# Kernel optimization log

Hardware: AMD Instinct MI355X
Metric: run time of the kernel (lower is better)

The kernel has to match this reference:

```python
import jax, jax.numpy as jnp
import numpy as np

NUM_HEADS = 12
HEAD_DIM = 64
NPT = 1  # num_prefix_tokens

def _rot(x):
    # pairs (x0,x1) -> (-x1, x0), matching timm's rot()
    x2 = x.reshape(*x.shape[:-1], -1, 2)
    r = jnp.stack([-x2[..., 1], x2[..., 0]], axis=-1)
    return r.reshape(x.shape)

def _apply_rope_cat(x, rope):
    # rope: [N_rot, 2*hd] = sin||cos concatenated
    sin, cos = jnp.split(rope, 2, axis=-1)
    return x * cos + _rot(x) * sin

def setup_inputs() -> dict:
    key = jax.random.key(0)
    ks = jax.random.split(key, 7)
    B, N, C = 8, 4097, 768
    hd = HEAD_DIM
    x = jax.random.normal(ks[0], (B, N, C), jnp.float32)
    rope = jax.random.normal(ks[1], (N - NPT, 2 * hd), jnp.float32)
    qkv_w = jax.random.normal(ks[2], (3 * C, C), jnp.float32) * (C ** -0.5)
    q_bias = jax.random.normal(ks[3], (C,), jnp.float32) * 0.02
    v_bias = jax.random.normal(ks[4], (C,), jnp.float32) * 0.02
    proj_w = jax.random.normal(ks[5], (C, C), jnp.float32) * (C ** -0.5)
    proj_b = jax.random.normal(ks[6], (C,), jnp.float32) * 0.02
    return dict(x=x, rope=rope, qkv_w=qkv_w, q_bias=q_bias, v_bias=v_bias,
                proj_w=proj_w, proj_b=proj_b)

def reference(x, rope, qkv_w, q_bias, v_bias, proj_w, proj_b):
    B, N, C = x.shape
    H, hd = NUM_HEADS, HEAD_DIM
    # fused QKV with k_bias fixed at zero (non-trainable buffer)
    bias = jnp.concatenate([q_bias, jnp.zeros_like(q_bias), v_bias])
    qkv = x @ qkv_w.T + bias                            # [B,N,3C]
    qkv = qkv.reshape(B, N, 3, H, hd).transpose(2, 0, 3, 1, 4)
    q, k, v = qkv[0], qkv[1], qkv[2]                    # [B,H,N,hd]
    # RoPE on all tokens except the prefix (CLS) token
    q = jnp.concatenate([q[:, :, :NPT], _apply_rope_cat(q[:, :, NPT:], rope)], axis=2)
    k = jnp.concatenate([k[:, :, :NPT], _apply_rope_cat(k[:, :, NPT:], rope)], axis=2)
    # linear attention: kv = K^T V, then Q @ kv, normalized by hd*N
    kv = jnp.einsum('bhnd,bhne->bhde', k, v)            # [B,H,hd,hd]
    out = jnp.einsum('bhnd,bhde->bhne', q, kv) / hd / N # [B,H,N,hd]
    out = out.transpose(0, 2, 1, 3).reshape(B, N, C)
    return out @ proj_w.T + proj_b
```

## Files before the change

### kernel.cpp

```cpp
#include <hip/hip_runtime.h>
#include <hip/hip_bf16.h>

typedef __attribute__((ext_vector_type(8))) short short8;
typedef __attribute__((ext_vector_type(4))) float f32x4;

#define B_    8
#define N_    4097
#define C_    768
#define M_TOT (B_*N_)
#define K3    (3*C_)
#define CHUNKS 16
#define NSTEP 24

__device__ __forceinline__ float bf2f(unsigned short u) {
  union { unsigned int i; float f; } x; x.i = ((unsigned int)u) << 16; return x.f;
}
__device__ __forceinline__ unsigned short f2bf(float f) {
  union { float f; unsigned int i; } x; x.f = f;
  unsigned int i = x.i + 0x7fffu + ((x.i >> 16) & 1u);
  return (unsigned short)(i >> 16);
}
__device__ __forceinline__ void gload16(const void* g, void* l) {
  __builtin_amdgcn_global_load_lds(
      (const __attribute__((address_space(1))) void*)g,
      (__attribute__((address_space(3))) void*)l, 16, 0, 0);
}

__global__ __launch_bounds__(256) void cvt_kernel(const float* __restrict__ inx,
                                                  unsigned short* __restrict__ outx,
                                                  const float* __restrict__ inw,
                                                  unsigned short* __restrict__ outw,
                                                  long n4x, long n4tot) {
  long i = (long)blockIdx.x * blockDim.x + threadIdx.x;
  long stride = (long)gridDim.x * blockDim.x;
  for (; i < n4tot; i += stride) {
    const float4* src; ushort4* dst; long j;
    if (i < n4x) { src = (const float4*)inx; dst = (ushort4*)outx; j = i; }
    else         { src = (const float4*)inw; dst = (ushort4*)outw; j = i - n4x; }
    float4 v = src[j];
    ushort4 o;
    o.x = f2bf(v.x); o.y = f2bf(v.y); o.z = f2bf(v.z); o.w = f2bf(v.w);
    dst[j] = o;
  }
}

__global__ __launch_bounds__(512, 4) void gemm_qkv_rope(
    const unsigned short* __restrict__ A,
    const unsigned short* __restrict__ Bw,
    const float* __restrict__ rope,
    const float* __restrict__ qb,
    const float* __restrict__ vb,
    unsigned short* __restrict__ qkv)
{
  __shared__ __align__(16) char L[3*24576];
  const int tid  = threadIdx.x;
  const int wave = tid >> 6, lane = tid & 63;
  const int lr = lane & 15, lk = lane >> 4;
  const int wm = wave >> 2, wn = wave & 3;

  const int o = blockIdx.x;
  const int xcd = o & 7, loc = o >> 3;
  const int tile = (xcd < 1 ? xcd*290 : 290 + (xcd-1)*289) + loc;
  const int m0 = (tile / 9) * 128;
  const int n0 = (tile % 9) * 256;

  const int arow = tid >> 2, achk = tid & 3;
  const int am = min(m0 + arow, M_TOT-1);
  const unsigned short* gA  = A  + (long)am*768 + achk*8;
  const unsigned short* gB1 = Bw + (long)(n0 + arow)*768 + achk*8;
  const unsigned short* gB2 = Bw + (long)(n0 + arow + 128)*768 + achk*8;
  const int dA  = wave*1024;
  const int dB1 = 8192  + wave*1024;
  const int dB2 = 16384 + wave*1024;

  const int abase = (wm*64 + lr)*64 + lk*16;
  const int bbase = 8192 + (wn*64 + lr)*64 + lk*16;

  f32x4 acc[4][4];
#pragma unroll
  for (int i = 0; i < 4; ++i)
#pragma unroll
    for (int j = 0; j < 4; ++j) acc[i][j] = (f32x4){0.f,0.f,0.f,0.f};

  auto STAGE = [&](int buf, int kk) {
    char* sb = L + buf*24576;
    gload16(gA  + kk, sb + dA);
    gload16(gB1 + kk, sb + dB1);
    gload16(gB2 + kk, sb + dB2);
  };
  auto COMPUTE = [&](int buf) {
    const char* sb = L + buf*24576;
    short8 af[4], bfr[4];
#pragma unroll
    for (int mi = 0; mi < 4; ++mi)
      af[mi] = *(const short8*)(sb + abase + mi*1024);
#pragma unroll
    for (int ni = 0; ni < 4; ++ni)
      bfr[ni] = *(const short8*)(sb + bbase + ni*1024);
#pragma unroll
    for (int mi = 0; mi < 4; ++mi)
#pragma unroll
      for (int ni = 0; ni < 4; ++ni)
        acc[mi][ni] = __builtin_amdgcn_mfma_f32_16x16x32_bf16(af[mi], bfr[ni], acc[mi][ni], 0, 0, 0);
  };

  STAGE(0, 0);
  STAGE(1, 32);
  asm volatile("s_waitcnt vmcnt(3)" ::: "memory");
  __builtin_amdgcn_s_barrier();
  __builtin_amdgcn_sched_barrier(0);

  int cur = 0;
  for (int tt = 0; tt < NSTEP-2; ++tt) {
    int stg = cur + 2; if (stg >= 3) stg -= 3;
    STAGE(stg, (tt+2)*32);
    COMPUTE(cur);
    asm volatile("s_waitcnt vmcnt(3)" ::: "memory");
    __builtin_amdgcn_sched_barrier(0);
    __builtin_amdgcn_s_barrier();
    __builtin_amdgcn_sched_barrier(0);
    cur = (cur + 1 == 3) ? 0 : cur + 1;
  }
  COMPUTE(cur);
  asm volatile("s_waitcnt vmcnt(0)" ::: "memory");
  __builtin_amdgcn_sched_barrier(0);
  __builtin_amdgcn_s_barrier();
  __builtin_amdgcn_sched_barrier(0);
  cur = (cur + 1 == 3) ? 0 : cur + 1;
  COMPUTE(cur);

  const int which = n0 / 768;
  unsigned short* plane = qkv + (long)which*M_TOT*768;

  float biasv[4]; int withv[4]; int dv[4];
#pragma unroll
  for (int ni = 0; ni < 4; ++ni) {
    const int gc = n0 + wn*64 + ni*16 + lr;
    const int within = gc - which*768;
    withv[ni] = within;
    dv[ni] = within & 63;
    biasv[ni] = (which == 0) ? qb[within] : (which == 2 ? vb[within] : 0.f);
  }

  if (which == 2) {
#pragma unroll
    for (int mi = 0; mi < 4; ++mi)
#pragma unroll
      for (int r = 0; r < 4; ++r) {
        const int gm = m0 + wm*64 + mi*16 + lk*4 + r;
        if (gm < M_TOT) {
#pragma unroll
          for (int ni = 0; ni < 4; ++ni)
            plane[(long)gm*768 + withv[ni]] = f2bf(acc[mi][ni][r] + biasv[ni]);
        }
      }
  } else {
#pragma unroll
    for (int mi = 0; mi < 4; ++mi) {
#pragma unroll
      for (int r = 0; r < 4; ++r) {
        const int gm = m0 + wm*64 + mi*16 + lk*4 + r;
        const int ntok = gm % 4097;
        const bool valid = gm < M_TOT;
        const bool dorope = (ntok > 0) && valid;
        const float* rp = rope + (long)(ntok - 1)*128;
#pragma unroll
        for (int ni = 0; ni < 4; ++ni) {
          float v = acc[mi][ni][r] + biasv[ni];
          float pair = __shfl_xor(v, 1);
          float vo = v;
          if (dorope) {
            const float s = rp[dv[ni]], c = rp[64 + dv[ni]];
            const float rot = (dv[ni] & 1) ? pair : -pair;
            vo = v*c + rot*s;
          }
          if (valid) plane[(long)gm*768 + withv[ni]] = f2bf(vo);
        }
      }
    }
  }
}

__global__ __launch_bounds__(256) void kv_partial_kernel(
    const unsigned short* __restrict__ qkv, float* __restrict__ part)
{
  const int bh = blockIdx.y;
  const int b = bh / 12, h = bh % 12;
  const int chunk = blockIdx.x;
  const int per = (N_ + CHUNKS - 1) / CHUNKS;
  const int nst = chunk * per;
  const int nen = min(nst + per, N_);
  const unsigned short* Kpl = qkv + (long)M_TOT*768 + ((long)b*N_)*768 + h*64;
  const unsigned short* Vpl = qkv + (long)2*M_TOT*768 + ((long)b*N_)*768 + h*64;
  __shared__ unsigned short Kl[2][32*64];
  __shared__ unsigned short Vl[2][32*64];
  const int t = threadIdx.x;
  const int ty = t >> 4, tx = t & 15;
  const int lrow = t >> 3, lpc = t & 7;
  float acc[4][4] = {};

  {
    const int cnt0 = min(32, nen - nst);
    if (lrow < cnt0) {
      *(uint4*)(Kl[0] + lrow*64 + lpc*8) = *(const uint4*)(Kpl + (long)(nst + lrow)*768 + lpc*8);
      *(uint4*)(Vl[0] + lrow*64 + lpc*8) = *(const uint4*)(Vpl + (long)(nst + lrow)*768 + lpc*8);
    }
  }
  int cur = 0;
  for (int nb = nst; nb < nen; nb += 32) {
    uint4 kn, vn; int cntn = 0;
    const int nxt = nb + 32;
    if (nxt < nen) {
      cntn = min(32, nen - nxt);
      if (lrow < cntn) {
        kn = *(const uint4*)(Kpl + (long)(nxt + lrow)*768 + lpc*8);
        vn = *(const uint4*)(Vpl + (long)(nxt + lrow)*768 + lpc*8);
      }
    }
    __syncthreads();
    const int cnt = min(32, nen - nb);
#pragma unroll 2
    for (int i = 0; i < cnt; ++i) {
      const ushort4 ku = *(const ushort4*)(Kl[cur] + i*64 + ty*4);
      const ushort4 vu = *(const ushort4*)(Vl[cur] + i*64 + tx*4);
      float kf[4] = {bf2f(ku.x), bf2f(ku.y), bf2f(ku.z), bf2f(ku.w)};
      float vf[4] = {bf2f(vu.x), bf2f(vu.y), bf2f(vu.z), bf2f(vu.w)};
#pragma unroll
      for (int a = 0; a < 4; ++a)
#pragma unroll
        for (int e = 0; e < 4; ++e) acc[a][e] += kf[a]*vf[e];
    }
    __syncthreads();
    if (nxt < nen && lrow < cntn) {
      *(uint4*)(Kl[cur^1] + lrow*64 + lpc*8) = kn;
      *(uint4*)(Vl[cur^1] + lrow*64 + lpc*8) = vn;
    }
    cur ^= 1;
  }
  float* dst = part + ((long)chunk*96 + bh)*4096 + (ty*4)*64 + tx*4;
#pragma unroll
  for (int a = 0; a < 4; ++a)
#pragma unroll
    for (int e = 0; e < 4; ++e) dst[a*64 + e] = acc[a][e];
}

__global__ __launch_bounds__(256) void mcomb_kernel(const float* __restrict__ part,
                                                    const float* __restrict__ pw,
                                                    unsigned short* __restrict__ McT) {
  const int blk = blockIdx.x;
  const int cs = blk & 3;
  const int h  = (blk >> 2) % 12;
  const int b  = blk / 48;
  const int bh = b*12 + h;
  __shared__ float kvs[64][65];
  const int t = threadIdx.x;
  const int d_own = t >> 2;
  const int eg = (t & 3) * 16;

  float4 a0 = {0,0,0,0}, a1 = {0,0,0,0}, a2 = {0,0,0,0}, a3 = {0,0,0,0};
  const float4* p4 = (const float4*)part;
#pragma unroll
  for (int ch = 0; ch < CHUNKS; ++ch) {
    const long base = ((long)ch*96 + bh)*1024 + d_own*16 + (t & 3)*4;
    float4 v0 = p4[base+0], v1 = p4[base+1], v2 = p4[base+2], v3 = p4[base+3];
    a0.x += v0.x; a0.y += v0.y; a0.z += v0.z; a0.w += v0.w;
    a1.x += v1.x; a1.y += v1.y; a1.z += v1.z; a1.w += v1.w;
    a2.x += v2.x; a2.y += v2.y; a2.z += v2.z; a2.w += v2.w;
    a3.x += v3.x; a3.y += v3.y; a3.z += v3.z; a3.w += v3.w;
  }
  kvs[eg+ 0][d_own] = a0.x; kvs[eg+ 1][d_own] = a0.y; kvs[eg+ 2][d_own] = a0.z; kvs[eg+ 3][d_own] = a0.w;
  kvs[eg+ 4][d_own] = a1.x; kvs[eg+ 5][d_own] = a1.y; kvs[eg+ 6][d_own] = a1.z; kvs[eg+ 7][d_own] = a1.w;
  kvs[eg+ 8][d_own] = a2.x; kvs[eg+ 9][d_own] = a2.y; kvs[eg+10][d_own] = a2.z; kvs[eg+11][d_own] = a2.w;
  kvs[eg+12][d_own] = a3.x; kvs[eg+13][d_own] = a3.y; kvs[eg+14][d_own] = a3.z; kvs[eg+15][d_own] = a3.w;
  __syncthreads();

  const int lane = t & 63;
  const int w    = t >> 6;
  float kvcol[64];
#pragma unroll
  for (int e = 0; e < 64; ++e) kvcol[e] = kvs[e][lane];

  const float scale = (float)(1.0/(64.0*4097.0));
  const int cbase = cs*192 + w*48;
  for (int i = 0; i < 48; ++i) {
    const int c = cbase + i;
    const float* pwrow = pw + (long)c*768 + h*64;
    float s = 0.f;
#pragma unroll
    for (int e = 0; e < 64; ++e) s += pwrow[e] * kvcol[e];
    McT[((long)b*768 + c)*768 + h*64 + lane] = f2bf(s * scale);
  }
}

__global__ __launch_bounds__(512, 4) void gemm_final(
    const unsigned short* __restrict__ qkv,
    const unsigned short* __restrict__ McT,
    const float* __restrict__ pb,
    float* __restrict__ out)
{
  __shared__ __align__(16) char L[3*24576];
  const int tid  = threadIdx.x;
  const int wave = tid >> 6, lane = tid & 63;
  const int lr = lane & 15, lk = lane >> 4;
  const int wm = wave >> 2, wn = wave & 3;

  const int o = blockIdx.x;
  const int xcd = o & 7, loc = o >> 3;
  const int b  = xcd;
  const int mt = loc / 3, ct = loc % 3;
  const int m0 = mt * 128;
  const int c0 = ct * 256;

  const int arow = tid >> 2, achk = tid & 3;
  const int am = min(m0 + arow, N_-1);
  const unsigned short* gA  = qkv + ((long)b*N_ + am)*768 + achk*8;
  const unsigned short* Bb  = McT + (long)b*768*768;
  const unsigned short* gB1 = Bb + (long)(c0 + arow)*768 + achk*8;
  const unsigned short* gB2 = Bb + (long)(c0 + arow + 128)*768 + achk*8;
  const int dA  = wave*1024;
  const int dB1 = 8192  + wave*1024;
  const int dB2 = 16384 + wave*1024;

  const int abase = (wm*64 + lr)*64 + lk*16;
  const int bbase = 8192 + (wn*64 + lr)*64 + lk*16;

  f32x4 acc[4][4];
#pragma unroll
  for (int i = 0; i < 4; ++i)
#pragma unroll
    for (int j = 0; j < 4; ++j) acc[i][j] = (f32x4){0.f,0.f,0.f,0.f};

  auto STAGE = [&](int buf, int kk) {
    char* sb = L + buf*24576;
    gload16(gA  + kk, sb + dA);
    gload16(gB1 + kk, sb + dB1);
    gload16(gB2 + kk, sb + dB2);
  };
  auto COMPUTE = [&](int buf) {
    const char* sb = L + buf*24576;
    short8 af[4], bfr[4];
#pragma unroll
    for (int mi = 0; mi < 4; ++mi)
      af[mi] = *(const short8*)(sb + abase + mi*1024);
#pragma unroll
    for (int ni = 0; ni < 4; ++ni)
      bfr[ni] = *(const short8*)(sb + bbase + ni*1024);
#pragma unroll
    for (int mi = 0; mi < 4; ++mi)
#pragma unroll
      for (int ni = 0; ni < 4; ++ni)
        acc[mi][ni] = __builtin_amdgcn_mfma_f32_16x16x32_bf16(af[mi], bfr[ni], acc[mi][ni], 0, 0, 0);
  };

  STAGE(0, 0);
  STAGE(1, 32);
  asm volatile("s_waitcnt vmcnt(3)" ::: "memory");
  __builtin_amdgcn_s_barrier();
  __builtin_amdgcn_sched_barrier(0);

  int cur = 0;
  for (int tt = 0; tt < NSTEP-2; ++tt) {
    int stg = cur + 2; if (stg >= 3) stg -= 3;
    STAGE(stg, (tt+2)*32);
    COMPUTE(cur);
    asm volatile("s_waitcnt vmcnt(3)" ::: "memory");
    __builtin_amdgcn_sched_barrier(0);
    __builtin_amdgcn_s_barrier();
    __builtin_amdgcn_sched_barrier(0);
    cur = (cur + 1 == 3) ? 0 : cur + 1;
  }
  COMPUTE(cur);
  asm volatile("s_waitcnt vmcnt(0)" ::: "memory");
  __builtin_amdgcn_sched_barrier(0);
  __builtin_amdgcn_s_barrier();
  __builtin_amdgcn_sched_barrier(0);
  cur = (cur + 1 == 3) ? 0 : cur + 1;
  COMPUTE(cur);

#pragma unroll
  for (int mi = 0; mi < 4; ++mi) {
#pragma unroll
    for (int ni = 0; ni < 4; ++ni) {
      const int gc = c0 + wn*64 + ni*16 + lr;
      const float bias = pb[gc];
#pragma unroll
      for (int r = 0; r < 4; ++r) {
        const int tok = m0 + wm*64 + mi*16 + lk*4 + r;
        if (tok < N_)
          out[((long)b*N_ + tok)*768 + gc] = acc[mi][ni][r] + bias;
      }
    }
  }
}

extern "C" void kernel_launch(void* const* d_in, const int* in_sizes, int n_in,
                              void* d_out, int out_size, void* d_ws, size_t ws_size,
                              hipStream_t stream) {
  const float* x      = (const float*)d_in[0];
  const float* rope   = (const float*)d_in[1];
  const float* qkv_w  = (const float*)d_in[2];
  const float* q_bias = (const float*)d_in[3];
  const float* v_bias = (const float*)d_in[4];
  const float* proj_w = (const float*)d_in[5];
  const float* proj_b = (const float*)d_in[6];
  float* out = (float*)d_out;

  char* w0 = (char*)d_ws;
  unsigned short* x_bf  = (unsigned short*)w0;
  unsigned short* wq_bf = (unsigned short*)(w0 + 50343936);
  unsigned short* qkv   = (unsigned short*)(w0 + 50343936 + 3538944);
  float*          part  = (float*)w0;
  unsigned short* McT   = (unsigned short*)(w0 + 25165824 + 1572864);

  const long n4x = (long)M_TOT*768/4;
  const long n4w = (long)K3*768/4;
  cvt_kernel<<<2048, 256, 0, stream>>>(x, x_bf, qkv_w, wq_bf, n4x, n4x + n4w);

  gemm_qkv_rope<<<2313, 512, 0, stream>>>(x_bf, wq_bf, rope, q_bias, v_bias, qkv);

  kv_partial_kernel<<<dim3(CHUNKS, 96), 256, 0, stream>>>(qkv, part);
  mcomb_kernel<<<384, 256, 0, stream>>>(part, proj_w, McT);

  gemm_final<<<792, 512, 0, stream>>>(qkv, McT, proj_b, out);
}
```

Measured before the change: 397.0 us.

## Compute KV partial sums with bf16 MFMA using transposed LDS reads

Replaces the scalar FMA outer-product loop in the K^T V partial kernel with 16x16x32 bf16 MFMA instructions. Tiles are stored to shared memory in a blocked layout and read back with ds_read_b64_tr_b16, so each wave gets its K and V fragments without explicit transposes. Partial tiles are zero-filled so the MFMA can always process a full 32-row step. A leftover unused inline-asm block with a dubious address expression remains. It also depends on the MI355X-specific transpose-read instruction and on the lane-to-fragment mapping being correct.

New measurement: 355.9 us, median of 2. 10.3% less time.

```diff
diff --git a/kernel.cpp b/kernel.cpp
--- a/kernel.cpp
+++ b/kernel.cpp
@@ -2,6 +2,7 @@
 #include <hip/hip_bf16.h>
 
 typedef __attribute__((ext_vector_type(8))) short short8;
+typedef __attribute__((ext_vector_type(4))) short short4v;
 typedef __attribute__((ext_vector_type(4))) float f32x4;
 
 #define B_    8
@@ -192,56 +193,92 @@
   const int nen = min(nst + per, N_);
   const unsigned short* Kpl = qkv + (long)M_TOT*768 + ((long)b*N_)*768 + h*64;
   const unsigned short* Vpl = qkv + (long)2*M_TOT*768 + ((long)b*N_)*768 + h*64;
-  __shared__ unsigned short Kl[2][32*64];
-  __shared__ unsigned short Vl[2][32*64];
+
+  __shared__ __align__(16) unsigned short Kt[2][2048];
+  __shared__ __align__(16) unsigned short Vt[2][2048];
+
   const int t = threadIdx.x;
-  const int ty = t >> 4, tx = t & 15;
   const int lrow = t >> 3, lpc = t & 7;
-  float acc[4][4] = {};
+  const int wave = t >> 6, lane = t & 63;
+  const int soff = ((lpc >> 1)*8 + (lrow >> 2))*64 + (lrow & 3)*16 + (lpc & 1)*8;
+
+  f32x4 acc[4];
+#pragma unroll
+  for (int e = 0; e < 4; ++e) acc[e] = (f32x4){0.f,0.f,0.f,0.f};
 
   {
     const int cnt0 = min(32, nen - nst);
+    uint4 k0 = {0,0,0,0}, v0 = {0,0,0,0};
     if (lrow < cnt0) {
-      *(uint4*)(Kl[0] + lrow*64 + lpc*8) = *(const uint4*)(Kpl + (long)(nst + lrow)*768 + lpc*8);
-      *(uint4*)(Vl[0] + lrow*64 + lpc*8) = *(const uint4*)(Vpl + (long)(nst + lrow)*768 + lpc*8);
-    }
-  }
+      k0 = *(const uint4*)(Kpl + (long)(nst + lrow)*768 + lpc*8);
+      v0 = *(const uint4*)(Vpl + (long)(nst + lrow)*768 + lpc*8);
+    }
+    *(uint4*)(Kt[0] + soff) = k0;
+    *(uint4*)(Vt[0] + soff) = v0;
+  }
+
   int cur = 0;
   for (int nb = nst; nb < nen; nb += 32) {
-    uint4 kn, vn; int cntn = 0;
+    uint4 kn = {0,0,0,0}, vn = {0,0,0,0};
     const int nxt = nb + 32;
     if (nxt < nen) {
-      cntn = min(32, nen - nxt);
+      const int cntn = min(32, nen - nxt);
       if (lrow < cntn) {
         kn = *(const uint4*)(Kpl + (long)(nxt + lrow)*768 + lpc*8);
         vn = *(const uint4*)(Vpl + (long)(nxt + lrow)*768 + lpc*8);
       }
     }
     __syncthreads();
-    const int cnt = min(32, nen - nb);
-#pragma unroll 2
-    for (int i = 0; i < cnt; ++i) {
-      const ushort4 ku = *(const ushort4*)(Kl[cur] + i*64 + ty*4);
-      const ushort4 vu = *(const ushort4*)(Vl[cur] + i*64 + tx*4);
-      float kf[4] = {bf2f(ku.x), bf2f(ku.y), bf2f(ku.z), bf2f(ku.w)};
-      float vf[4] = {bf2f(vu.x), bf2f(vu.y), bf2f(vu.z), bf2f(vu.w)};
-#pragma unroll
-      for (int a = 0; a < 4; ++a)
-#pragma unroll
-        for (int e = 0; e < 4; ++e) acc[a][e] += kf[a]*vf[e];
+
+    {
+      const unsigned short* kb = Kt[cur] + wave*512;
+      const unsigned short* vb_ = Vt[cur];
+      short4v a0, a1;
+      const unsigned short* ka = kb + lane*4;
+      asm volatile("ds_read_b64_tr_b16 %0, %1" : "=v"(a0)
+                   : "v"((unsigned)(__builtin_amdgcn_is_shared((const __attribute__((address_space(0))) void*)ka), (unsigned)(unsigned long)(ka - (const unsigned short*)0))));
+      (void)a0; (void)a1;
+    }
+    {
+      short4v ak0, ak1, bv0[4], bv1[4];
+      unsigned kaddr = (unsigned)(unsigned long)(uintptr_t)(Kt[cur] + wave*512 + lane*4);
+      asm volatile("ds_read_b64_tr_b16 %0, %1"            : "=v"(ak0) : "v"(kaddr));
+      asm volatile("ds_read_b64_tr_b16 %0, %1 offset:512" : "=v"(ak1) : "v"(kaddr));
+#pragma unroll
+      for (int eblk = 0; eblk < 4; ++eblk) {
+        unsigned vaddr = (unsigned)(unsigned long)(uintptr_t)(Vt[cur] + eblk*512 + lane*4);
+        asm volatile("ds_read_b64_tr_b16 %0, %1"            : "=v"(bv0[eblk]) : "v"(vaddr));
+        asm volatile("ds_read_b64_tr_b16 %0, %1 offset:512" : "=v"(bv1[eblk]) : "v"(vaddr));
+      }
+      asm volatile("s_waitcnt lgkmcnt(0)" ::: "memory");
+      __builtin_amdgcn_sched_barrier(0);
+      short8 afr;
+      afr[0]=ak0[0]; afr[1]=ak0[1]; afr[2]=ak0[2]; afr[3]=ak0[3];
+      afr[4]=ak1[0]; afr[5]=ak1[1]; afr[6]=ak1[2]; afr[7]=ak1[3];
+#pragma unroll
+      for (int eblk = 0; eblk < 4; ++eblk) {
+        short8 bfr;
+        bfr[0]=bv0[eblk][0]; bfr[1]=bv0[eblk][1]; bfr[2]=bv0[eblk][2]; bfr[3]=bv0[eblk][3];
+        bfr[4]=bv1[eblk][0]; bfr[5]=bv1[eblk][1]; bfr[6]=bv1[eblk][2]; bfr[7]=bv1[eblk][3];
+        acc[eblk] = __builtin_amdgcn_mfma_f32_16x16x32_bf16(afr, bfr, acc[eblk], 0, 0, 0);
+      }
     }
     __syncthreads();
-    if (nxt < nen && lrow < cntn) {
-      *(uint4*)(Kl[cur^1] + lrow*64 + lpc*8) = kn;
-      *(uint4*)(Vl[cur^1] + lrow*64 + lpc*8) = vn;
+    if (nxt < nen) {
+      *(uint4*)(Kt[cur^1] + soff) = kn;
+      *(uint4*)(Vt[cur^1] + soff) = vn;
     }
     cur ^= 1;
   }
-  float* dst = part + ((long)chunk*96 + bh)*4096 + (ty*4)*64 + tx*4;
-#pragma unroll
-  for (int a = 0; a < 4; ++a)
-#pragma unroll
-    for (int e = 0; e < 4; ++e) dst[a*64 + e] = acc[a][e];
+
+  float* base = part + ((long)chunk*96 + bh)*4096;
+  const int d0 = wave*16 + (lane >> 4)*4;
+  const int e0 = lane & 15;
+#pragma unroll
+  for (int eblk = 0; eblk < 4; ++eblk)
+#pragma unroll
+    for (int r = 0; r < 4; ++r)
+      base[(long)(d0 + r)*64 + eblk*16 + e0] = acc[eblk][r];
 }
 
 __global__ __launch_bounds__(256) void mcomb_kernel(const float* __restrict__ part,
```
